# Kernel optimization log

Measured on AMD Instinct MI355X. Metric: run time of the kernel, lower is better.

The kernel has to match this reference:

```python
import jax, jax.numpy as jnp
import numpy as np

N_NODES = 50000
N_EDGES = 800000
D_IN = 128
D_OUT = 128


def setup_inputs() -> dict:
    key = jax.random.key(0)
    ks = jax.random.split(key, 10)
    x = jax.random.normal(ks[0], (N_NODES, D_IN), dtype=jnp.float32)
    src = jax.random.randint(ks[1], (N_EDGES,), 0, N_NODES, dtype=jnp.int32)
    dst = jax.random.randint(ks[2], (N_EDGES,), 0, N_NODES, dtype=jnp.int32)
    s = 1.0 / np.sqrt(D_IN)
    def lin(k, din, dout):
        kw, kb = jax.random.split(k)
        W = jax.random.uniform(kw, (din, dout), minval=-s, maxval=s, dtype=jnp.float32)
        b = jax.random.uniform(kb, (dout,), minval=-s, maxval=s, dtype=jnp.float32)
        return W, b
    W1, b1 = lin(ks[3], D_IN, D_IN)
    W2, b2 = lin(ks[4], D_IN, D_IN)
    W3, b3 = lin(ks[5], D_IN, D_OUT)
    return dict(x=x, W1=W1, b1=b1, W2=W2, b2=b2, W3=W3, b3=b3, src=src, dst=dst)


def reference(x, W1, b1, W2, b2, W3, b3, src, dst):
    n = x.shape[0]
    ones = jnp.ones(src.shape[0], dtype=x.dtype)
    in_deg = jax.ops.segment_sum(ones, dst, num_segments=n)    # [N]
    out_deg = jax.ops.segment_sum(ones, src, num_segments=n)   # [N]

    def sage_gcn(h, W, b):
        # DGL SAGEConv(aggregator_type='gcn'), eval mode (feat_drop = identity):
        # h_neigh = (sum_{j in N(i)} h_j + h_i) / (in_deg_i + 1); out = h_neigh @ W + b
        neigh = jax.ops.segment_sum(h[src], dst, num_segments=n)  # [N, D]
        h_neigh = (neigh + h) / (in_deg + 1.0)[:, None]
        return h_neigh @ W + b

    h = sage_gcn(x, W1, b1)
    h = sage_gcn(h, W2, b2)

    # DGL GraphConv norm='both', allow_zero_in_degree=True:
    # out = D_in^{-1/2} A D_out^{-1/2} h W + b, degrees clamped to >= 1
    norm_out = jnp.clip(out_deg, 1.0) ** -0.5
    norm_in = jnp.clip(in_deg, 1.0) ** -0.5
    hs = h * norm_out[:, None]
    agg = jax.ops.segment_sum(hs[src], dst, num_segments=n)
    out = (agg * norm_in[:, None]) @ W3 + b3
    return out
```

## Files before the change

### kernel.cpp

```cpp
#include <hip/hip_runtime.h>

#define NN 50000
#define NE 800000
#define D 128

#define CH 32
#define EPC (NE / CH)
#define RGH 4
#define NPRH (NN / RGH)
#define CSRCAP (NE + 16 * NN)

#define HIST_BLOCKS (CH * RGH)
#define CVT_BLOCKS 1563
#define WT_BLOCKS 48

typedef short bf16x8 __attribute__((ext_vector_type(8)));
typedef float f32x4 __attribute__((ext_vector_type(4)));


__device__ __forceinline__ unsigned bf16rne(float f) {
  unsigned u = __float_as_uint(f);
  return (u + 0x7fffu + ((u >> 16) & 1u)) >> 16;
}
__device__ __forceinline__ unsigned packbf(float lo, float hi) {
  return bf16rne(lo) | (bf16rne(hi) << 16);
}

__global__ __launch_bounds__(1024) void cvtw_hist_kernel(
    const float* __restrict__ x, const float* __restrict__ W1,
    const float* __restrict__ W2, const float* __restrict__ W3,
    unsigned short* __restrict__ hbf, unsigned short* __restrict__ T1,
    unsigned short* __restrict__ T2, unsigned short* __restrict__ T3,
    const int* __restrict__ src, const int* __restrict__ dst,
    int* __restrict__ partial_dst, int* __restrict__ partial_src) {
  __shared__ int hd[NPRH];
  __shared__ int hs[NPRH];
  int b = blockIdx.x;
  int tid = threadIdx.x;
  if (b < HIST_BLOCKS) {
    int c = b >> 2;
    int r = b & 3;
    int base = r * NPRH;
    for (int i = tid; i < NPRH; i += 1024) { hd[i] = 0; hs[i] = 0; }
    __syncthreads();
    int e0 = c * EPC;
    for (int i = tid; i < EPC; i += 1024) {
      int d = dst[e0 + i];
      int s = src[e0 + i];
      unsigned dr = (unsigned)(d - base);
      unsigned sr = (unsigned)(s - base);
      if (dr < NPRH) atomicAdd(&hd[dr], 1);
      if (sr < NPRH) atomicAdd(&hs[sr], 1);
    }
    __syncthreads();
    for (int i = tid; i < NPRH; i += 1024) {
      partial_dst[c * NN + base + i] = hd[i];
      partial_src[c * NN + base + i] = hs[i];
    }
  } else if (b < HIST_BLOCKS + CVT_BLOCKS) {
    int i = (b - HIST_BLOCKS) * 1024 + tid;
    if (i < NN * D / 4) {
      float4 v = ((const float4*)x)[i];
      uint2 p;
      p.x = packbf(v.x, v.y);
      p.y = packbf(v.z, v.w);
      ((uint2*)hbf)[i] = p;
    }
  } else if (b < HIST_BLOCKS + CVT_BLOCKS + WT_BLOCKS) {
    int g = b - (HIST_BLOCKS + CVT_BLOCKS);
    int w = g >> 4;
    int i = (g & 15) * 1024 + tid;
    const float* W = (w == 0) ? W1 : (w == 1) ? W2 : W3;
    unsigned short* T = (w == 0) ? T1 : (w == 1) ? T2 : T3;
    int n = i >> 7, k = i & 127;
    T[n * 128 + k] = (unsigned short)bf16rne(W[k * 128 + n]);
  } else {
    if (tid < 16) ((uint4*)(hbf + (size_t)NN * D))[tid] = make_uint4(0, 0, 0, 0);
  }
}

__device__ __forceinline__ int block_excl_scan(int v, int* wsum) {
  int lane = threadIdx.x & 63;
  int w = threadIdx.x >> 6;
  int incl = v;
#pragma unroll
  for (int off = 1; off < 64; off <<= 1) {
    int t = __shfl_up(incl, off);
    if (lane >= off) incl += t;
  }
  if (lane == 63) wsum[w] = incl;
  __syncthreads();
  int wo = 0;
#pragma unroll
  for (int j = 0; j < 4; ++j)
    if (j < w) wo += wsum[j];
  return wo + incl - v;
}

__global__ __launch_bounds__(256) void degscan_kernel(int* __restrict__ partial_dst,
                                                      const int* __restrict__ partial_src,
                                                      int* __restrict__ degtmp,
                                                      int* __restrict__ deg_out,
                                                      int* __restrict__ row_ptr,
                                                      int* __restrict__ partials, int N) {
  __shared__ int wsum[4];
  int d = blockIdx.x * 256 + threadIdx.x;
  int run = 0;
  if (d < N) {
#pragma unroll
    for (int c = 0; c < CH; ++c) {
      int v = partial_dst[c * NN + d];
      partial_dst[c * NN + d] = run;
      run += v;
    }
    degtmp[d] = run;
    int ro = 0;
#pragma unroll
    for (int c = 0; c < CH; ++c) ro += partial_src[c * NN + d];
    deg_out[d] = ro;
  }
  int pad = (run + 3) & ~3;
  int excl = block_excl_scan(pad, wsum);
  if (d <= N) row_ptr[d] = excl;
  if (threadIdx.x == 255) partials[blockIdx.x] = excl + pad;
}

__global__ __launch_bounds__(256) void scan2(int* __restrict__ partials, int nb) {
  __shared__ int wsum[4];
  int v = (threadIdx.x < nb) ? partials[threadIdx.x] : 0;
  int excl = block_excl_scan(v, wsum);
  if (threadIdx.x < nb) partials[threadIdx.x] = excl;
}

__global__ __launch_bounds__(1024) void fill_kernel(const int* __restrict__ src,
                                                    const int* __restrict__ dst,
                                                    const int* __restrict__ row_ptr,
                                                    const int* __restrict__ partials,
                                                    const int* __restrict__ partial_dst,
                                                    int* __restrict__ csr_src) {
  __shared__ int cur[NPRH];
  int tid = threadIdx.x;
  int c = blockIdx.x >> 2;
  int r = blockIdx.x & 3;
  int base = r * NPRH;
  for (int i = tid; i < NPRH; i += 1024) {
    int nd = base + i;
    cur[i] = row_ptr[nd] + partials[nd >> 8] + partial_dst[c * NN + nd];
  }
  __syncthreads();
  int e0 = c * EPC;
  for (int i = tid; i < EPC; i += 1024) {
    int d = dst[e0 + i];
    unsigned dr = (unsigned)(d - base);
    if (dr < NPRH) {
      int pos = atomicAdd(&cur[dr], 1);
      csr_src[pos] = src[e0 + i];
    }
  }
  if (c == CH - 1) {
    __syncthreads();
    for (int i = tid; i < NPRH; i += 1024) {
      int nd = base + i;
      int s = cur[i];
      int e = row_ptr[nd + 1] + partials[(nd + 1) >> 8];
      for (int j = s; j < e; ++j) csr_src[j] = NN;
    }
  }
}

__device__ __forceinline__ void bacc(float* a, uint4 u) {
  a[0] += __uint_as_float(u.x << 16);
  a[1] += __uint_as_float(u.x & 0xffff0000u);
  a[2] += __uint_as_float(u.y << 16);
  a[3] += __uint_as_float(u.y & 0xffff0000u);
  a[4] += __uint_as_float(u.z << 16);
  a[5] += __uint_as_float(u.z & 0xffff0000u);
  a[6] += __uint_as_float(u.w << 16);
  a[7] += __uint_as_float(u.w & 0xffff0000u);
}

template <int MODE>
__global__ __launch_bounds__(256, 8) void agg_kernel(const unsigned short* __restrict__ hb,
                                                     const int* __restrict__ row_ptr,
                                                     const int* __restrict__ partials,
                                                     const int* __restrict__ csr_src,
                                                     const int* __restrict__ degtmp,
                                                     unsigned short* __restrict__ outb, int N) {
  int qw = threadIdx.x >> 4;
  int col = threadIdx.x & 15;
  int node = blockIdx.x * 16 + qw;
  if (node >= N) return;
  int start = row_ptr[node] + partials[node >> 8];
  int end = row_ptr[node + 1] + partials[(node + 1) >> 8];
  int indeg = degtmp[node];
  uint4 srow = make_uint4(0, 0, 0, 0);
  if (MODE == 0) srow = ((const uint4*)(hb + (size_t)node * D))[col];
  float a0[8] = {0, 0, 0, 0, 0, 0, 0, 0};
  float a1[8] = {0, 0, 0, 0, 0, 0, 0, 0};
  const int* ce = csr_src + start;
  int cnt = end - start;
  for (int it = 0; it < cnt; it += 4) {
    int4 ix = *(const int4*)(ce + it);
    uint4 u0 = ((const uint4*)(hb + (size_t)ix.x * D))[col];
    uint4 u1 = ((const uint4*)(hb + (size_t)ix.y * D))[col];
    uint4 u2 = ((const uint4*)(hb + (size_t)ix.z * D))[col];
    uint4 u3 = ((const uint4*)(hb + (size_t)ix.w * D))[col];
    bacc(a0, u0);
    bacc(a1, u1);
    bacc(a0, u2);
    bacc(a1, u3);
  }
#pragma unroll
  for (int j = 0; j < 8; ++j) a0[j] += a1[j];
  if (MODE == 0) {
    float sf[8] = {0, 0, 0, 0, 0, 0, 0, 0};
    bacc(sf, srow);
    float inv = 1.0f / (float)(indeg + 1);
#pragma unroll
    for (int j = 0; j < 8; ++j) a0[j] = (a0[j] + sf[j]) * inv;
  } else {
    float sc = rsqrtf(fmaxf((float)indeg, 1.0f));
#pragma unroll
    for (int j = 0; j < 8; ++j) a0[j] *= sc;
  }
  uint4 p;
  p.x = packbf(a0[0], a0[1]);
  p.y = packbf(a0[2], a0[3]);
  p.z = packbf(a0[4], a0[5]);
  p.w = packbf(a0[6], a0[7]);
  ((uint4*)(outb + (size_t)node * D))[col] = p;
}

template <int MODE, int OUT_BF>
__global__ __launch_bounds__(256) void mgemm_kernel(const unsigned short* __restrict__ A,
                                                    const unsigned short* __restrict__ WT,
                                                    const float* __restrict__ bias,
                                                    const int* __restrict__ deg_out,
                                                    float* __restrict__ outf,
                                                    unsigned short* __restrict__ outb, int N) {
  __shared__ unsigned short sWT[128 * 136];
  int tid = threadIdx.x;
  for (int g = tid; g < 2048; g += 256) {
    int n = g >> 4, c = g & 15;
    uint4 v = ((const uint4*)WT)[g];
    *(uint4*)&sWT[n * 136 + c * 8] = v;
  }
  int wv = tid >> 6;
  int lane = tid & 63;
  int q = lane >> 4;
  int ln = lane & 15;
  int row0 = blockIdx.x * 64 + wv * 16;
  int arow = row0 + ln;
  if (arow >= N) arow = 0;
  const unsigned short* Ar = A + (size_t)arow * 128 + q * 8;
  bf16x8 af0 = *(const bf16x8*)(Ar + 0);
  bf16x8 af1 = *(const bf16x8*)(Ar + 32);
  bf16x8 af2 = *(const bf16x8*)(Ar + 64);
  bf16x8 af3 = *(const bf16x8*)(Ar + 96);
  f32x4 acc[8];
#pragma unroll
  for (int t = 0; t < 8; ++t) acc[t] = (f32x4){0.f, 0.f, 0.f, 0.f};
  __syncthreads();
#pragma unroll
  for (int t = 0; t < 8; ++t) {
    const unsigned short* Wr = &sWT[(t * 16 + ln) * 136 + q * 8];
    bf16x8 b0 = *(const bf16x8*)(Wr + 0);
    bf16x8 b1 = *(const bf16x8*)(Wr + 32);
    bf16x8 b2 = *(const bf16x8*)(Wr + 64);
    bf16x8 b3 = *(const bf16x8*)(Wr + 96);
    acc[t] = __builtin_amdgcn_mfma_f32_16x16x32_bf16(af0, b0, acc[t], 0, 0, 0);
    acc[t] = __builtin_amdgcn_mfma_f32_16x16x32_bf16(af1, b1, acc[t], 0, 0, 0);
    acc[t] = __builtin_amdgcn_mfma_f32_16x16x32_bf16(af2, b2, acc[t], 0, 0, 0);
    acc[t] = __builtin_amdgcn_mfma_f32_16x16x32_bf16(af3, b3, acc[t], 0, 0, 0);
  }
  float scl[4];
#pragma unroll
  for (int r = 0; r < 4; ++r) {
    scl[r] = 1.0f;
    if (MODE == 1) {
      int row = row0 + q * 4 + r;
      int rr = (row < N) ? row : 0;
      scl[r] = rsqrtf(fmaxf((float)deg_out[rr], 1.0f));
    }
  }
#pragma unroll
  for (int t = 0; t < 8; ++t) {
    float b = bias[t * 16 + ln];
#pragma unroll
    for (int r = 0; r < 4; ++r) {
      int row = row0 + q * 4 + r;
      if (row < N) {
        float v = (acc[t][r] + b) * scl[r];
        if (OUT_BF)
          outb[(size_t)row * 128 + t * 16 + ln] = (unsigned short)bf16rne(v);
        else
          outf[(size_t)row * 128 + t * 16 + ln] = v;
      }
    }
  }
}


extern "C" void kernel_launch(void* const* d_in, const int* in_sizes, int n_in,
                              void* d_out, int out_size, void* d_ws, size_t ws_size,
                              hipStream_t stream) {
  const float* x = (const float*)d_in[0];
  const float* W1 = (const float*)d_in[1];
  const float* b1 = (const float*)d_in[2];
  const float* W2 = (const float*)d_in[3];
  const float* b2 = (const float*)d_in[4];
  const float* W3 = (const float*)d_in[5];
  const float* b3 = (const float*)d_in[6];
  const int* src = (const int*)d_in[7];
  const int* dst = (const int*)d_in[8];
  float* out = (float*)d_out;

  const int N = NN;

  unsigned short* hbf = (unsigned short*)d_ws;
  unsigned short* aggB = hbf + (size_t)(NN + 1) * D;
  unsigned short* WT1 = aggB + (size_t)NN * D;
  unsigned short* WT2 = WT1 + D * D;
  unsigned short* WT3 = WT2 + D * D;
  int* partial_dst = (int*)(WT3 + D * D);
  int* partial_src = partial_dst + (size_t)CH * NN;
  int* degtmp = partial_src + (size_t)CH * NN;
  int* deg_out = degtmp + NN;
  int* row_ptr = deg_out + NN;
  int* partials = row_ptr + NN + 1;
  int* csr_src = partials + 256;

  const int scanBlocks = (N + 255) / 256;

  cvtw_hist_kernel<<<HIST_BLOCKS + CVT_BLOCKS + WT_BLOCKS + 1, 1024, 0, stream>>>(
      x, W1, W2, W3, hbf, WT1, WT2, WT3, src, dst, partial_dst, partial_src);
  degscan_kernel<<<scanBlocks, 256, 0, stream>>>(partial_dst, partial_src, degtmp,
                                                 deg_out, row_ptr, partials, N);
  scan2<<<1, 256, 0, stream>>>(partials, scanBlocks);
  fill_kernel<<<CH * RGH, 1024, 0, stream>>>(src, dst, row_ptr, partials, partial_dst,
                                             csr_src);

  int aggBlocks = (N + 15) / 16;
  int gemmBlocks = (N + 63) / 64;

  agg_kernel<0><<<aggBlocks, 256, 0, stream>>>(hbf, row_ptr, partials, csr_src, degtmp,
                                               aggB, N);
  mgemm_kernel<0, 1><<<gemmBlocks, 256, 0, stream>>>(aggB, WT1, b1, deg_out, nullptr, hbf, N);
  agg_kernel<0><<<aggBlocks, 256, 0, stream>>>(hbf, row_ptr, partials, csr_src, degtmp,
                                               aggB, N);
  mgemm_kernel<1, 1><<<gemmBlocks, 256, 0, stream>>>(aggB, WT2, b2, deg_out, nullptr, hbf, N);
  agg_kernel<1><<<aggBlocks, 256, 0, stream>>>(hbf, row_ptr, partials, csr_src, degtmp,
                                               aggB, N);
  mgemm_kernel<0, 0><<<gemmBlocks, 256, 0, stream>>>(aggB, WT3, b3, deg_out, out, nullptr, N);
}
```

Before: 260.9 us.

## Fuse neighbor aggregation with MFMA GEMM per layer using ping-pong buffers

Merges each aggregation kernel with the following dense transform, so aggregated rows are staged in shared memory and multiplied by the transposed weights within one block. Two bf16 feature buffers replace the separate aggregate buffer, which removes three launches and one global round trip of the aggregated matrix per layer. The cost is that only 2 of 8 waves run the MFMA phase, the full weight tile is reloaded into LDS by every 32-node block, and larger LDS use may limit occupancy during the latency-bound gather. CSRCAP shrinks and the partials offset is realigned.

```diff
diff --git a/kernel.cpp b/kernel.cpp
--- a/kernel.cpp
+++ b/kernel.cpp
@@ -8,7 +8,7 @@
 #define EPC (NE / CH)
 #define RGH 4
 #define NPRH (NN / RGH)
-#define CSRCAP (NE + 16 * NN)
+#define CSRCAP (NE + 4 * NN)
 
 #define HIST_BLOCKS (CH * RGH)
 #define CVT_BLOCKS 1563
@@ -25,14 +25,25 @@
 __device__ __forceinline__ unsigned packbf(float lo, float hi) {
   return bf16rne(lo) | (bf16rne(hi) << 16);
 }
+__device__ __forceinline__ void bacc(float* a, uint4 u) {
+  a[0] += __uint_as_float(u.x << 16);
+  a[1] += __uint_as_float(u.x & 0xffff0000u);
+  a[2] += __uint_as_float(u.y << 16);
+  a[3] += __uint_as_float(u.y & 0xffff0000u);
+  a[4] += __uint_as_float(u.z << 16);
+  a[5] += __uint_as_float(u.z & 0xffff0000u);
+  a[6] += __uint_as_float(u.w << 16);
+  a[7] += __uint_as_float(u.w & 0xffff0000u);
+}
 
 __global__ __launch_bounds__(1024) void cvtw_hist_kernel(
     const float* __restrict__ x, const float* __restrict__ W1,
     const float* __restrict__ W2, const float* __restrict__ W3,
-    unsigned short* __restrict__ hbf, unsigned short* __restrict__ T1,
-    unsigned short* __restrict__ T2, unsigned short* __restrict__ T3,
-    const int* __restrict__ src, const int* __restrict__ dst,
-    int* __restrict__ partial_dst, int* __restrict__ partial_src) {
+    unsigned short* __restrict__ h0, unsigned short* __restrict__ h1,
+    unsigned short* __restrict__ T1, unsigned short* __restrict__ T2,
+    unsigned short* __restrict__ T3, const int* __restrict__ src,
+    const int* __restrict__ dst, int* __restrict__ partial_dst,
+    int* __restrict__ partial_src) {
   __shared__ int hd[NPRH];
   __shared__ int hs[NPRH];
   int b = blockIdx.x;
@@ -64,7 +75,7 @@
       uint2 p;
       p.x = packbf(v.x, v.y);
       p.y = packbf(v.z, v.w);
-      ((uint2*)hbf)[i] = p;
+      ((uint2*)h0)[i] = p;
     }
   } else if (b < HIST_BLOCKS + CVT_BLOCKS + WT_BLOCKS) {
     int g = b - (HIST_BLOCKS + CVT_BLOCKS);
@@ -75,7 +86,10 @@
     int n = i >> 7, k = i & 127;
     T[n * 128 + k] = (unsigned short)bf16rne(W[k * 128 + n]);
   } else {
-    if (tid < 16) ((uint4*)(hbf + (size_t)NN * D))[tid] = make_uint4(0, 0, 0, 0);
+    if (tid < 16) {
+      ((uint4*)(h0 + (size_t)NN * D))[tid] = make_uint4(0, 0, 0, 0);
+      ((uint4*)(h1 + (size_t)NN * D))[tid] = make_uint4(0, 0, 0, 0);
+    }
   }
 }
 
@@ -168,133 +182,118 @@
   }
 }
 
-__device__ __forceinline__ void bacc(float* a, uint4 u) {
-  a[0] += __uint_as_float(u.x << 16);
-  a[1] += __uint_as_float(u.x & 0xffff0000u);
-  a[2] += __uint_as_float(u.y << 16);
-  a[3] += __uint_as_float(u.y & 0xffff0000u);
-  a[4] += __uint_as_float(u.z << 16);
-  a[5] += __uint_as_float(u.z & 0xffff0000u);
-  a[6] += __uint_as_float(u.w << 16);
-  a[7] += __uint_as_float(u.w & 0xffff0000u);
-}
-
-template <int MODE>
-__global__ __launch_bounds__(256, 8) void agg_kernel(const unsigned short* __restrict__ hb,
-                                                     const int* __restrict__ row_ptr,
-                                                     const int* __restrict__ partials,
-                                                     const int* __restrict__ csr_src,
-                                                     const int* __restrict__ degtmp,
-                                                     unsigned short* __restrict__ outb, int N) {
-  int qw = threadIdx.x >> 4;
-  int col = threadIdx.x & 15;
-  int node = blockIdx.x * 16 + qw;
-  if (node >= N) return;
-  int start = row_ptr[node] + partials[node >> 8];
-  int end = row_ptr[node + 1] + partials[(node + 1) >> 8];
-  int indeg = degtmp[node];
-  uint4 srow = make_uint4(0, 0, 0, 0);
-  if (MODE == 0) srow = ((const uint4*)(hb + (size_t)node * D))[col];
-  float a0[8] = {0, 0, 0, 0, 0, 0, 0, 0};
-  float a1[8] = {0, 0, 0, 0, 0, 0, 0, 0};
-  const int* ce = csr_src + start;
-  int cnt = end - start;
-  for (int it = 0; it < cnt; it += 4) {
-    int4 ix = *(const int4*)(ce + it);
-    uint4 u0 = ((const uint4*)(hb + (size_t)ix.x * D))[col];
-    uint4 u1 = ((const uint4*)(hb + (size_t)ix.y * D))[col];
-    uint4 u2 = ((const uint4*)(hb + (size_t)ix.z * D))[col];
-    uint4 u3 = ((const uint4*)(hb + (size_t)ix.w * D))[col];
-    bacc(a0, u0);
-    bacc(a1, u1);
-    bacc(a0, u2);
-    bacc(a1, u3);
-  }
-#pragma unroll
-  for (int j = 0; j < 8; ++j) a0[j] += a1[j];
-  if (MODE == 0) {
-    float sf[8] = {0, 0, 0, 0, 0, 0, 0, 0};
-    bacc(sf, srow);
-    float inv = 1.0f / (float)(indeg + 1);
-#pragma unroll
-    for (int j = 0; j < 8; ++j) a0[j] = (a0[j] + sf[j]) * inv;
-  } else {
-    float sc = rsqrtf(fmaxf((float)indeg, 1.0f));
-#pragma unroll
-    for (int j = 0; j < 8; ++j) a0[j] *= sc;
-  }
-  uint4 p;
-  p.x = packbf(a0[0], a0[1]);
-  p.y = packbf(a0[2], a0[3]);
-  p.z = packbf(a0[4], a0[5]);
-  p.w = packbf(a0[6], a0[7]);
-  ((uint4*)(outb + (size_t)node * D))[col] = p;
-}
-
-template <int MODE, int OUT_BF>
-__global__ __launch_bounds__(256) void mgemm_kernel(const unsigned short* __restrict__ A,
-                                                    const unsigned short* __restrict__ WT,
-                                                    const float* __restrict__ bias,
-                                                    const int* __restrict__ deg_out,
-                                                    float* __restrict__ outf,
-                                                    unsigned short* __restrict__ outb, int N) {
+template <int MODE_AGG, int MODE_SCALE, int OUT_BF>
+__global__ __launch_bounds__(512, 4) void fused_kernel(
+    const unsigned short* __restrict__ tin, const int* __restrict__ row_ptr,
+    const int* __restrict__ partials, const int* __restrict__ csr_src,
+    const int* __restrict__ degtmp, const int* __restrict__ deg_out,
+    const unsigned short* __restrict__ WT, const float* __restrict__ bias,
+    unsigned short* __restrict__ outb, float* __restrict__ outf, int N) {
   __shared__ unsigned short sWT[128 * 136];
+  __shared__ unsigned short sA[32 * 136];
   int tid = threadIdx.x;
-  for (int g = tid; g < 2048; g += 256) {
+  for (int g = tid; g < 2048; g += 512) {
     int n = g >> 4, c = g & 15;
     uint4 v = ((const uint4*)WT)[g];
     *(uint4*)&sWT[n * 136 + c * 8] = v;
   }
-  int wv = tid >> 6;
-  int lane = tid & 63;
-  int q = lane >> 4;
-  int ln = lane & 15;
-  int row0 = blockIdx.x * 64 + wv * 16;
-  int arow = row0 + ln;
-  if (arow >= N) arow = 0;
-  const unsigned short* Ar = A + (size_t)arow * 128 + q * 8;
-  bf16x8 af0 = *(const bf16x8*)(Ar + 0);
-  bf16x8 af1 = *(const bf16x8*)(Ar + 32);
-  bf16x8 af2 = *(const bf16x8*)(Ar + 64);
-  bf16x8 af3 = *(const bf16x8*)(Ar + 96);
-  f32x4 acc[8];
-#pragma unroll
-  for (int t = 0; t < 8; ++t) acc[t] = (f32x4){0.f, 0.f, 0.f, 0.f};
+  int qw = tid >> 4;
+  int col = tid & 15;
+  int nb = blockIdx.x * 32;
+  int node = nb + qw;
+  float a0[8] = {0, 0, 0, 0, 0, 0, 0, 0};
+  float a1[8] = {0, 0, 0, 0, 0, 0, 0, 0};
+  if (node < N) {
+    int start = row_ptr[node] + partials[node >> 8];
+    int end = row_ptr[node + 1] + partials[(node + 1) >> 8];
+    int indeg = degtmp[node];
+    uint4 srow = make_uint4(0, 0, 0, 0);
+    if (MODE_AGG == 0) srow = ((const uint4*)(tin + (size_t)node * D))[col];
+    const int* ce = csr_src + start;
+    int cnt = end - start;
+    for (int it = 0; it < cnt; it += 4) {
+      int4 ix = *(const int4*)(ce + it);
+      uint4 u0 = ((const uint4*)(tin + (size_t)ix.x * D))[col];
+      uint4 u1 = ((const uint4*)(tin + (size_t)ix.y * D))[col];
+      uint4 u2 = ((const uint4*)(tin + (size_t)ix.z * D))[col];
+      uint4 u3 = ((const uint4*)(tin + (size_t)ix.w * D))[col];
+      bacc(a0, u0);
+      bacc(a1, u1);
+      bacc(a0, u2);
+      bacc(a1, u3);
+    }
+#pragma unroll
+    for (int j = 0; j < 8; ++j) a0[j] += a1[j];
+    if (MODE_AGG == 0) {
+      float sf[8] = {0, 0, 0, 0, 0, 0, 0, 0};
+      bacc(sf, srow);
+      float inv = 1.0f / (float)(indeg + 1);
+#pragma unroll
+      for (int j = 0; j < 8; ++j) a0[j] = (a0[j] + sf[j]) * inv;
+    } else {
+      float sc = rsqrtf(fmaxf((float)indeg, 1.0f));
+#pragma unroll
+      for (int j = 0; j < 8; ++j) a0[j] *= sc;
+    }
+  }
+  {
+    uint4 p;
+    p.x = packbf(a0[0], a0[1]);
+    p.y = packbf(a0[2], a0[3]);
+    p.z = packbf(a0[4], a0[5]);
+    p.w = packbf(a0[6], a0[7]);
+    *(uint4*)&sA[qw * 136 + col * 8] = p;
+  }
   __syncthreads();
-#pragma unroll
-  for (int t = 0; t < 8; ++t) {
-    const unsigned short* Wr = &sWT[(t * 16 + ln) * 136 + q * 8];
-    bf16x8 b0 = *(const bf16x8*)(Wr + 0);
-    bf16x8 b1 = *(const bf16x8*)(Wr + 32);
-    bf16x8 b2 = *(const bf16x8*)(Wr + 64);
-    bf16x8 b3 = *(const bf16x8*)(Wr + 96);
-    acc[t] = __builtin_amdgcn_mfma_f32_16x16x32_bf16(af0, b0, acc[t], 0, 0, 0);
-    acc[t] = __builtin_amdgcn_mfma_f32_16x16x32_bf16(af1, b1, acc[t], 0, 0, 0);
-    acc[t] = __builtin_amdgcn_mfma_f32_16x16x32_bf16(af2, b2, acc[t], 0, 0, 0);
-    acc[t] = __builtin_amdgcn_mfma_f32_16x16x32_bf16(af3, b3, acc[t], 0, 0, 0);
-  }
-  float scl[4];
-#pragma unroll
-  for (int r = 0; r < 4; ++r) {
-    scl[r] = 1.0f;
-    if (MODE == 1) {
-      int row = row0 + q * 4 + r;
-      int rr = (row < N) ? row : 0;
-      scl[r] = rsqrtf(fmaxf((float)deg_out[rr], 1.0f));
-    }
-  }
-#pragma unroll
-  for (int t = 0; t < 8; ++t) {
-    float b = bias[t * 16 + ln];
+  if (tid < 128) {
+    int wv = tid >> 6;
+    int lane = tid & 63;
+    int q = lane >> 4;
+    int ln = lane & 15;
+    int row0 = nb + wv * 16;
+    const unsigned short* Ar = &sA[(wv * 16 + ln) * 136 + q * 8];
+    bf16x8 af0 = *(const bf16x8*)(Ar + 0);
+    bf16x8 af1 = *(const bf16x8*)(Ar + 32);
+    bf16x8 af2 = *(const bf16x8*)(Ar + 64);
+    bf16x8 af3 = *(const bf16x8*)(Ar + 96);
+    f32x4 acc[8];
+#pragma unroll
+    for (int t = 0; t < 8; ++t) acc[t] = (f32x4){0.f, 0.f, 0.f, 0.f};
+#pragma unroll
+    for (int t = 0; t < 8; ++t) {
+      const unsigned short* Wr = &sWT[(t * 16 + ln) * 136 + q * 8];
+      bf16x8 b0 = *(const bf16x8*)(Wr + 0);
+      bf16x8 b1 = *(const bf16x8*)(Wr + 32);
+      bf16x8 b2 = *(const bf16x8*)(Wr + 64);
+      bf16x8 b3 = *(const bf16x8*)(Wr + 96);
+      acc[t] = __builtin_amdgcn_mfma_f32_16x16x32_bf16(af0, b0, acc[t], 0, 0, 0);
+      acc[t] = __builtin_amdgcn_mfma_f32_16x16x32_bf16(af1, b1, acc[t], 0, 0, 0);
+      acc[t] = __builtin_amdgcn_mfma_f32_16x16x32_bf16(af2, b2, acc[t], 0, 0, 0);
+      acc[t] = __builtin_amdgcn_mfma_f32_16x16x32_bf16(af3, b3, acc[t], 0, 0, 0);
+    }
+    float scl[4];
 #pragma unroll
     for (int r = 0; r < 4; ++r) {
-      int row = row0 + q * 4 + r;
-      if (row < N) {
-        float v = (acc[t][r] + b) * scl[r];
-        if (OUT_BF)
-          outb[(size_t)row * 128 + t * 16 + ln] = (unsigned short)bf16rne(v);
-        else
-          outf[(size_t)row * 128 + t * 16 + ln] = v;
+      scl[r] = 1.0f;
+      if (MODE_SCALE == 1) {
+        int row = row0 + q * 4 + r;
+        int rr = (row < N) ? row : 0;
+        scl[r] = rsqrtf(fmaxf((float)deg_out[rr], 1.0f));
+      }
+    }
+#pragma unroll
+    for (int t = 0; t < 8; ++t) {
+      float b = bias[t * 16 + ln];
+#pragma unroll
+      for (int r = 0; r < 4; ++r) {
+        int row = row0 + q * 4 + r;
+        if (row < N) {
+          float v = (acc[t][r] + b) * scl[r];
+          if (OUT_BF)
+            outb[(size_t)row * 128 + t * 16 + ln] = (unsigned short)bf16rne(v);
+          else
+            outf[(size_t)row * 128 + t * 16 + ln] = v;
+        }
       }
     }
   }
@@ -317,9 +316,9 @@
 
   const int N = NN;
 
-  unsigned short* hbf = (unsigned short*)d_ws;
-  unsigned short* aggB = hbf + (size_t)(NN + 1) * D;
-  unsigned short* WT1 = aggB + (size_t)NN * D;
+  unsigned short* h0 = (unsigned short*)d_ws;
+  unsigned short* h1 = h0 + (size_t)(NN + 1) * D;
+  unsigned short* WT1 = h1 + (size_t)(NN + 1) * D;
   unsigned short* WT2 = WT1 + D * D;
   unsigned short* WT3 = WT2 + D * D;
   int* partial_dst = (int*)(WT3 + D * D);
@@ -327,29 +326,25 @@
   int* degtmp = partial_src + (size_t)CH * NN;
   int* deg_out = degtmp + NN;
   int* row_ptr = deg_out + NN;
-  int* partials = row_ptr + NN + 1;
+  int* partials = row_ptr + NN + 4;
   int* csr_src = partials + 256;
 
   const int scanBlocks = (N + 255) / 256;
 
   cvtw_hist_kernel<<<HIST_BLOCKS + CVT_BLOCKS + WT_BLOCKS + 1, 1024, 0, stream>>>(
-      x, W1, W2, W3, hbf, WT1, WT2, WT3, src, dst, partial_dst, partial_src);
+      x, W1, W2, W3, h0, h1, WT1, WT2, WT3, src, dst, partial_dst, partial_src);
   degscan_kernel<<<scanBlocks, 256, 0, stream>>>(partial_dst, partial_src, degtmp,
                                                  deg_out, row_ptr, partials, N);
   scan2<<<1, 256, 0, stream>>>(partials, scanBlocks);
   fill_kernel<<<CH * RGH, 1024, 0, stream>>>(src, dst, row_ptr, partials, partial_dst,
                                              csr_src);
 
-  int aggBlocks = (N + 15) / 16;
-  int gemmBlocks = (N + 63) / 64;
-
-  agg_kernel<0><<<aggBlocks, 256, 0, stream>>>(hbf, row_ptr, partials, csr_src, degtmp,
-                                               aggB, N);
-  mgemm_kernel<0, 1><<<gemmBlocks, 256, 0, stream>>>(aggB, WT1, b1, deg_out, nullptr, hbf, N);
-  agg_kernel<0><<<aggBlocks, 256, 0, stream>>>(hbf, row_ptr, partials, csr_src, degtmp,
-                                               aggB, N);
-  mgemm_kernel<1, 1><<<gemmBlocks, 256, 0, stream>>>(aggB, WT2, b2, deg_out, nullptr, hbf, N);
-  agg_kernel<1><<<aggBlocks, 256, 0, stream>>>(hbf, row_ptr, partials, csr_src, degtmp,
-                                               aggB, N);
-  mgemm_kernel<0, 0><<<gemmBlocks, 256, 0, stream>>>(aggB, WT3, b3, deg_out, out, nullptr, N);
-}
+  int layerBlocks = (N + 31) / 32;
+
+  fused_kernel<0, 0, 1><<<layerBlocks, 512, 0, stream>>>(
+      h0, row_ptr, partials, csr_src, degtmp, deg_out, WT1, b1, h1, nullptr, N);
+  fused_kernel<0, 1, 1><<<layerBlocks, 512, 0, stream>>>(
+      h1, row_ptr, partials, csr_src, degtmp, deg_out, WT2, b2, h0, nullptr, N);
+  fused_kernel<1, 0, 0><<<layerBlocks, 512, 0, stream>>>(
+      h0, row_ptr, partials, csr_src, degtmp, deg_out, WT3, b3, nullptr, out, N);
+}
```

Result: slower. 276.6 us (+6.0%).

## Pack dst/src histogram counts into one word and use more edge chunks

Applied to the files above, without the earlier changes.

The histogram now packs in-degree (low 16 bits) and out-degree (high 16 bits) into a single shared-memory counter per node. That halves LDS use, so each block covers half the node range (RGH=2) and there are 128 edge chunks instead of 32. Per-chunk prefix offsets are stored as 16-bit values and the aggregation buffer aliases the partial-histogram storage, which shrinks workspace traffic. The cost is a longer per-node scan loop over 128 chunks, and the packing assumes per-chunk counts stay below 65536.

```diff
diff --git a/kernel.cpp b/kernel.cpp
--- a/kernel.cpp
+++ b/kernel.cpp
@@ -4,11 +4,11 @@
 #define NE 800000
 #define D 128
 
-#define CH 32
+#define CH 128
 #define EPC (NE / CH)
-#define RGH 4
-#define NPRH (NN / RGH)
-#define CSRCAP (NE + 16 * NN)
+#define RGH 2
+#define NPR2 (NN / RGH)
+#define CSRCAP (NE + 4 * NN)
 
 #define HIST_BLOCKS (CH * RGH)
 #define CVT_BLOCKS 1563
@@ -25,23 +25,32 @@
 __device__ __forceinline__ unsigned packbf(float lo, float hi) {
   return bf16rne(lo) | (bf16rne(hi) << 16);
 }
-
-__global__ __launch_bounds__(1024) void cvtw_hist_kernel(
+__device__ __forceinline__ void bacc(float* a, uint4 u) {
+  a[0] += __uint_as_float(u.x << 16);
+  a[1] += __uint_as_float(u.x & 0xffff0000u);
+  a[2] += __uint_as_float(u.y << 16);
+  a[3] += __uint_as_float(u.y & 0xffff0000u);
+  a[4] += __uint_as_float(u.z << 16);
+  a[5] += __uint_as_float(u.z & 0xffff0000u);
+  a[6] += __uint_as_float(u.w << 16);
+  a[7] += __uint_as_float(u.w & 0xffff0000u);
+}
+
+__global__ __launch_bounds__(1024) void prep_kernel(
     const float* __restrict__ x, const float* __restrict__ W1,
     const float* __restrict__ W2, const float* __restrict__ W3,
     unsigned short* __restrict__ hbf, unsigned short* __restrict__ T1,
     unsigned short* __restrict__ T2, unsigned short* __restrict__ T3,
     const int* __restrict__ src, const int* __restrict__ dst,
-    int* __restrict__ partial_dst, int* __restrict__ partial_src) {
-  __shared__ int hd[NPRH];
-  __shared__ int hs[NPRH];
+    unsigned* __restrict__ partial) {
+  __shared__ unsigned hcnt[NPR2];
   int b = blockIdx.x;
   int tid = threadIdx.x;
   if (b < HIST_BLOCKS) {
-    int c = b >> 2;
-    int r = b & 3;
-    int base = r * NPRH;
-    for (int i = tid; i < NPRH; i += 1024) { hd[i] = 0; hs[i] = 0; }
+    int c = b >> 1;
+    int r = b & 1;
+    int base = r * NPR2;
+    for (int i = tid; i < NPR2; i += 1024) hcnt[i] = 0;
     __syncthreads();
     int e0 = c * EPC;
     for (int i = tid; i < EPC; i += 1024) {
@@ -49,14 +58,12 @@
       int s = src[e0 + i];
       unsigned dr = (unsigned)(d - base);
       unsigned sr = (unsigned)(s - base);
-      if (dr < NPRH) atomicAdd(&hd[dr], 1);
-      if (sr < NPRH) atomicAdd(&hs[sr], 1);
+      if (dr < NPR2) atomicAdd(&hcnt[dr], 1u);
+      if (sr < NPR2) atomicAdd(&hcnt[sr], 0x10000u);
     }
     __syncthreads();
-    for (int i = tid; i < NPRH; i += 1024) {
-      partial_dst[c * NN + base + i] = hd[i];
-      partial_src[c * NN + base + i] = hs[i];
-    }
+    for (int i = tid; i < NPR2; i += 1024)
+      partial[(size_t)c * NN + base + i] = hcnt[i];
   } else if (b < HIST_BLOCKS + CVT_BLOCKS) {
     int i = (b - HIST_BLOCKS) * 1024 + tid;
     if (i < NN * D / 4) {
@@ -97,26 +104,24 @@
   return wo + incl - v;
 }
 
-__global__ __launch_bounds__(256) void degscan_kernel(int* __restrict__ partial_dst,
-                                                      const int* __restrict__ partial_src,
+__global__ __launch_bounds__(256) void degscan_kernel(const unsigned* __restrict__ partial,
+                                                      unsigned short* __restrict__ pofs,
                                                       int* __restrict__ degtmp,
                                                       int* __restrict__ deg_out,
                                                       int* __restrict__ row_ptr,
                                                       int* __restrict__ partials, int N) {
   __shared__ int wsum[4];
   int d = blockIdx.x * 256 + threadIdx.x;
-  int run = 0;
+  int run = 0, ro = 0;
   if (d < N) {
-#pragma unroll
+#pragma unroll 8
     for (int c = 0; c < CH; ++c) {
-      int v = partial_dst[c * NN + d];
-      partial_dst[c * NN + d] = run;
-      run += v;
+      unsigned v = partial[(size_t)c * NN + d];
+      pofs[(size_t)c * NN + d] = (unsigned short)run;
+      run += (int)(v & 0xffffu);
+      ro += (int)(v >> 16);
     }
     degtmp[d] = run;
-    int ro = 0;
-#pragma unroll
-    for (int c = 0; c < CH; ++c) ro += partial_src[c * NN + d];
     deg_out[d] = ro;
   }
   int pad = (run + 3) & ~3;
@@ -136,47 +141,36 @@
                                                     const int* __restrict__ dst,
                                                     const int* __restrict__ row_ptr,
                                                     const int* __restrict__ partials,
-                                                    const int* __restrict__ partial_dst,
+                                                    const unsigned short* __restrict__ pofs,
                                                     int* __restrict__ csr_src) {
-  __shared__ int cur[NPRH];
+  __shared__ int cur[NPR2];
   int tid = threadIdx.x;
-  int c = blockIdx.x >> 2;
-  int r = blockIdx.x & 3;
-  int base = r * NPRH;
-  for (int i = tid; i < NPRH; i += 1024) {
+  int c = blockIdx.x >> 1;
+  int r = blockIdx.x & 1;
+  int base = r * NPR2;
+  for (int i = tid; i < NPR2; i += 1024) {
     int nd = base + i;
-    cur[i] = row_ptr[nd] + partials[nd >> 8] + partial_dst[c * NN + nd];
+    cur[i] = row_ptr[nd] + partials[nd >> 8] + (int)pofs[(size_t)c * NN + nd];
   }
   __syncthreads();
   int e0 = c * EPC;
   for (int i = tid; i < EPC; i += 1024) {
     int d = dst[e0 + i];
     unsigned dr = (unsigned)(d - base);
-    if (dr < NPRH) {
+    if (dr < NPR2) {
       int pos = atomicAdd(&cur[dr], 1);
       csr_src[pos] = src[e0 + i];
     }
   }
   if (c == CH - 1) {
     __syncthreads();
-    for (int i = tid; i < NPRH; i += 1024) {
+    for (int i = tid; i < NPR2; i += 1024) {
       int nd = base + i;
       int s = cur[i];
       int e = row_ptr[nd + 1] + partials[(nd + 1) >> 8];
       for (int j = s; j < e; ++j) csr_src[j] = NN;
     }
   }
-}
-
-__device__ __forceinline__ void bacc(float* a, uint4 u) {
-  a[0] += __uint_as_float(u.x << 16);
-  a[1] += __uint_as_float(u.x & 0xffff0000u);
-  a[2] += __uint_as_float(u.y << 16);
-  a[3] += __uint_as_float(u.y & 0xffff0000u);
-  a[4] += __uint_as_float(u.z << 16);
-  a[5] += __uint_as_float(u.z & 0xffff0000u);
-  a[6] += __uint_as_float(u.w << 16);
-  a[7] += __uint_as_float(u.w & 0xffff0000u);
 }
 
 template <int MODE>
@@ -318,27 +312,27 @@
   const int N = NN;
 
   unsigned short* hbf = (unsigned short*)d_ws;
-  unsigned short* aggB = hbf + (size_t)(NN + 1) * D;
-  unsigned short* WT1 = aggB + (size_t)NN * D;
+  unsigned short* WT1 = hbf + (size_t)(NN + 1) * D;
   unsigned short* WT2 = WT1 + D * D;
   unsigned short* WT3 = WT2 + D * D;
-  int* partial_dst = (int*)(WT3 + D * D);
-  int* partial_src = partial_dst + (size_t)CH * NN;
-  int* degtmp = partial_src + (size_t)CH * NN;
+  int* degtmp = (int*)(WT3 + D * D);
   int* deg_out = degtmp + NN;
   int* row_ptr = deg_out + NN;
-  int* partials = row_ptr + NN + 1;
+  int* partials = row_ptr + NN + 4;
   int* csr_src = partials + 256;
+  unsigned* partial = (unsigned*)(csr_src + CSRCAP);
+  unsigned short* pofs = (unsigned short*)(partial + (size_t)CH * NN);
+  unsigned short* aggB = (unsigned short*)partial;
 
   const int scanBlocks = (N + 255) / 256;
 
-  cvtw_hist_kernel<<<HIST_BLOCKS + CVT_BLOCKS + WT_BLOCKS + 1, 1024, 0, stream>>>(
-      x, W1, W2, W3, hbf, WT1, WT2, WT3, src, dst, partial_dst, partial_src);
-  degscan_kernel<<<scanBlocks, 256, 0, stream>>>(partial_dst, partial_src, degtmp,
-                                                 deg_out, row_ptr, partials, N);
+  prep_kernel<<<HIST_BLOCKS + CVT_BLOCKS + WT_BLOCKS + 1, 1024, 0, stream>>>(
+      x, W1, W2, W3, hbf, WT1, WT2, WT3, src, dst, partial);
+  degscan_kernel<<<scanBlocks, 256, 0, stream>>>(partial, pofs, degtmp, deg_out,
+                                                 row_ptr, partials, N);
   scan2<<<1, 256, 0, stream>>>(partials, scanBlocks);
-  fill_kernel<<<CH * RGH, 1024, 0, stream>>>(src, dst, row_ptr, partials, partial_dst,
-                                             csr_src);
+  fill_kernel<<<HIST_BLOCKS, 1024, 0, stream>>>(src, dst, row_ptr, partials, pofs,
+                                                csr_src);
 
   int aggBlocks = (N + 15) / 16;
   int gemmBlocks = (N + 63) / 64;
```

New measurement: 268.0 us. 1.03x slower.
